# Performance work log

Measured on AMD Instinct MI355X. Metric: run time of the kernel, lower is better.

## Reference

```python
import jax, jax.numpy as jnp
import numpy as np
import math

D = 512          # model_dim
H = 8            # num_heads
HD = D // H      # head_dim
L = 6            # num_layers
FF = 2 * D       # dim_feedforward
IN_DIM = 24
MAX_LEN = 1024   # positional_embedding_dim (sinusoidal max_len)
NUM_CLASSES = 1
B, S = 8, 1024
EPS = 1e-5


def make_sinusoidal_pe(max_len, d_model):
    position = np.arange(max_len, dtype=np.float32)[:, None]
    div_term = np.exp(np.arange(0, d_model, 2, dtype=np.float32) * (-math.log(10000.0) / d_model))
    pe = np.zeros((max_len, d_model), dtype=np.float32)
    pe[:, 0::2] = np.sin(position * div_term)
    pe[:, 1::2] = np.cos(position * div_term)
    return jnp.asarray(pe)


def layer_norm(x, g, b):
    mu = jnp.mean(x, axis=-1, keepdims=True)
    var = jnp.mean(jnp.square(x - mu), axis=-1, keepdims=True)
    return (x - mu) * jax.lax.rsqrt(var + EPS) * g + b


def setup_inputs() -> dict:
    key = jax.random.key(0)
    ks = jax.random.split(key, 16)
    xavier = lambda k, shape: jax.random.uniform(
        k, shape, jnp.float32,
        -math.sqrt(6.0 / (shape[-2] + shape[-1])),
        math.sqrt(6.0 / (shape[-2] + shape[-1])))
    inp = {
        'x': jax.random.normal(ks[0], (B, S, IN_DIM), jnp.float32),
        'positions': jax.random.randint(ks[1], (B, S), 0, MAX_LEN),
        'pe': make_sinusoidal_pe(MAX_LEN, D),
        'input_W': xavier(ks[2], (IN_DIM, D)),
        'input_b': jnp.zeros((D,), jnp.float32),
        'qkv_W': xavier(ks[3], (L, D, 3 * D)),
        'qkv_b': jnp.zeros((L, 3 * D), jnp.float32),
        'o_W': xavier(ks[4], (L, D, D)),
        'o_b': jnp.zeros((L, D), jnp.float32),
        'ff1_W': xavier(ks[5], (L, D, FF)),
        'ff1_b': jnp.zeros((L, FF), jnp.float32),
        'ff2_W': xavier(ks[6], (L, FF, D)),
        'ff2_b': jnp.zeros((L, D), jnp.float32),
        'ln1_g': jnp.ones((L, D), jnp.float32),
        'ln1_b': jnp.zeros((L, D), jnp.float32),
        'ln2_g': jnp.ones((L, D), jnp.float32),
        'ln2_b': jnp.zeros((L, D), jnp.float32),
        'out1_W': xavier(ks[7], (D, D)),
        'out1_b': jnp.zeros((D,), jnp.float32),
        'outln_g': jnp.ones((D,), jnp.float32),
        'outln_b': jnp.zeros((D,), jnp.float32),
        'out2_W': xavier(ks[8], (D, NUM_CLASSES)),
        'out2_b': jnp.zeros((NUM_CLASSES,), jnp.float32),
    }
    return inp


def reference(x, positions, pe, input_W, input_b, qkv_W, qkv_b, o_W, o_b,
              ff1_W, ff1_b, ff2_W, ff2_b, ln1_g, ln1_b, ln2_g, ln2_b,
              out1_W, out1_b, outln_g, outln_b, out2_W, out2_b):
    b, s, _ = x.shape
    # input projection + sinusoidal positional encoding gathered at positions
    h = x @ input_W + input_b + pe[positions]            # [B,S,D]
    scale = 1.0 / math.sqrt(HD)
    for l in range(qkv_W.shape[0]):
        qkv = (h @ qkv_W[l] + qkv_b[l]).reshape(b, s, H, 3 * HD)
        q = jnp.transpose(qkv[..., :HD], (0, 2, 1, 3))           # [B,H,S,hd]
        k = jnp.transpose(qkv[..., HD:2 * HD], (0, 2, 1, 3))
        v = jnp.transpose(qkv[..., 2 * HD:], (0, 2, 1, 3))
        logits = jnp.einsum('bhqd,bhkd->bhqk', q, k) * scale     # [B,H,S,S]
        attn = jax.nn.softmax(logits, axis=-1)
        vals = jnp.einsum('bhqk,bhkd->bhqd', attn, v)
        vals = jnp.transpose(vals, (0, 2, 1, 3)).reshape(b, s, D)
        attn_out = vals @ o_W[l] + o_b[l]
        h = layer_norm(h + attn_out, ln1_g[l], ln1_b[l])
        ff = jax.nn.relu(h @ ff1_W[l] + ff1_b[l]) @ ff2_W[l] + ff2_b[l]
        h = layer_norm(h + ff, ln2_g[l], ln2_b[l])
    pooled = jnp.mean(h, axis=1)                                 # [B,D] mean pooling
    o = jax.nn.relu(layer_norm(pooled @ out1_W + out1_b, outln_g, outln_b))
    return o @ out2_W + out2_b                                   # [B,num_classes]
```

## Files before the change

### kernel.cpp

```cpp
#include <hip/hip_runtime.h>
#include <cstddef>

#define EPS 1e-5f

typedef short bf16x8 __attribute__((ext_vector_type(8)));
typedef float f32x4 __attribute__((ext_vector_type(4)));
typedef unsigned short u16x8 __attribute__((ext_vector_type(8)));
typedef unsigned short u16x4 __attribute__((ext_vector_type(4)));

__device__ __forceinline__ unsigned short f2bf(float x) {
  unsigned u = __float_as_uint(x);
  return (unsigned short)((u + 0x7FFFu + ((u >> 16) & 1u)) >> 16);
}

__device__ __forceinline__ void gl2lds16(const unsigned short* g, unsigned short* l) {
  __builtin_amdgcn_global_load_lds(
      (const __attribute__((address_space(1))) unsigned int*)g,
      (__attribute__((address_space(3))) unsigned int*)l, 16, 0, 0);
}

__global__ __launch_bounds__(512) void inproj_kernel(
    const float* __restrict__ x, const int* __restrict__ pos,
    const float* __restrict__ pe, const float* __restrict__ Wp,
    const float* __restrict__ bp, float* __restrict__ h,
    unsigned short* __restrict__ hb) {
  int t = blockIdx.x, d = threadIdx.x;
  __shared__ float xs[24];
  if (d < 24) xs[d] = x[(size_t)t * 24 + d];
  __syncthreads();
  float acc = bp[d] + pe[(size_t)pos[t] * 512 + d];
#pragma unroll
  for (int k = 0; k < 24; ++k) acc += xs[k] * Wp[k * 512 + d];
  h[(size_t)t * 512 + d] = acc;
  hb[(size_t)t * 512 + d] = f2bf(acc);
}

__global__ __launch_bounds__(256) void wcast_kernel(
    const float* __restrict__ qw, const float* __restrict__ ow,
    const float* __restrict__ f1w, const float* __restrict__ f2w,
    unsigned short* __restrict__ qd, unsigned short* __restrict__ od,
    unsigned short* __restrict__ f1d, unsigned short* __restrict__ f2d) {
  __shared__ float sm[64][65];
  int bid = blockIdx.x;
  const float* src; unsigned short* dst; int K, N, tile;
  if (bid < 192)      { src = qw;  dst = qd;  K = 512;  N = 1536; tile = bid; }
  else if (bid < 256) { src = ow;  dst = od;  K = 512;  N = 512;  tile = bid - 192; }
  else if (bid < 384) { src = f1w; dst = f1d; K = 512;  N = 1024; tile = bid - 256; }
  else                { src = f2w; dst = f2d; K = 1024; N = 512;  tile = bid - 384; }
  int nt = N >> 6;
  int tk = tile / nt, tn = tile % nt;
  int k0 = tk * 64, n0 = tn * 64;
  int tid = threadIdx.x;
#pragma unroll
  for (int it = 0; it < 16; ++it) {
    int idx = it * 256 + tid;
    int ki = idx >> 6, ni = idx & 63;
    sm[ki][ni] = src[(size_t)(k0 + ki) * N + n0 + ni];
  }
  __syncthreads();
#pragma unroll
  for (int it = 0; it < 16; ++it) {
    int idx = it * 256 + tid;
    int ni = idx >> 6, ki = idx & 63;
    dst[(size_t)(n0 + ni) * K + k0 + ki] = f2bf(sm[ki][ni]);
  }
}

template <int MODE>
__global__ __launch_bounds__(256) void gemm_bf16(
    const unsigned short* __restrict__ A, const unsigned short* __restrict__ Bw,
    const float* __restrict__ bias, float* __restrict__ Cf,
    unsigned short* __restrict__ Cb, unsigned short* __restrict__ q_out,
    unsigned short* __restrict__ k_out, unsigned short* __restrict__ v_out,
    int M, int N, int K) {
  __shared__ unsigned short As[128 * 64];
  __shared__ unsigned short Bs[128 * 64];
  int tid = threadIdx.x;
  int w = tid >> 6, l = tid & 63;
  int wm = w >> 1, wn = w & 1;
  int cl = l & 15, kg = l >> 4;
  int n0 = blockIdx.x * 128, m0 = blockIdx.y * 128;
  f32x4 acc[4][4];
#pragma unroll
  for (int i = 0; i < 4; ++i)
#pragma unroll
    for (int j = 0; j < 4; ++j) acc[i][j] = f32x4{0.f, 0.f, 0.f, 0.f};

  const unsigned short* Ap = A + (size_t)m0 * K;
  const unsigned short* Bp = Bw + (size_t)n0 * K;

  for (int k0 = 0; k0 < K; k0 += 64) {
    __syncthreads();
#pragma unroll
    for (int c = 0; c < 4; ++c) {
      int idx = c * 256 + tid;
      int r = idx >> 3;
      int kq = (idx & 7) ^ (r & 7);
      gl2lds16(Ap + (size_t)r * K + k0 + kq * 8, &As[(c * 256 + w * 64) * 8]);
    }
#pragma unroll
    for (int c = 0; c < 4; ++c) {
      int idx = c * 256 + tid;
      int r = idx >> 3;
      int kq = (idx & 7) ^ (r & 7);
      gl2lds16(Bp + (size_t)r * K + k0 + kq * 8, &Bs[(c * 256 + w * 64) * 8]);
    }
    __syncthreads();
    bf16x8 af[4][2], bfr[4][2];
    int key = (cl & 7) << 4;
#pragma unroll
    for (int i = 0; i < 4; ++i) {
      int rowa = wm * 64 + i * 16 + cl;
      int rowb = wn * 64 + i * 16 + cl;
#pragma unroll
      for (int s2 = 0; s2 < 2; ++s2) {
        af[i][s2]  = *(const bf16x8*)((char*)As + ((rowa * 128 + s2 * 64 + kg * 16) ^ key));
        bfr[i][s2] = *(const bf16x8*)((char*)Bs + ((rowb * 128 + s2 * 64 + kg * 16) ^ key));
      }
    }
#pragma unroll
    for (int i = 0; i < 4; ++i)
#pragma unroll
      for (int j = 0; j < 4; ++j) {
        acc[i][j] = __builtin_amdgcn_mfma_f32_16x16x32_bf16(af[i][0], bfr[j][0], acc[i][j], 0, 0, 0);
        acc[i][j] = __builtin_amdgcn_mfma_f32_16x16x32_bf16(af[i][1], bfr[j][1], acc[i][j], 0, 0, 0);
      }
  }

  int rl = kg * 4;
#pragma unroll
  for (int i = 0; i < 4; ++i) {
    int mbase = m0 + wm * 64 + i * 16 + rl;
#pragma unroll
    for (int j = 0; j < 4; ++j) {
      int col = n0 + wn * 64 + j * 16 + cl;
      float bv = bias[col];
      if (MODE == 0) {
#pragma unroll
        for (int r = 0; r < 4; ++r)
          Cf[(size_t)(mbase + r) * N + col] = acc[i][j][r] + bv;
      } else if (MODE == 1) {
#pragma unroll
        for (int r = 0; r < 4; ++r)
          Cb[(size_t)(mbase + r) * N + col] = f2bf(fmaxf(acc[i][j][r] + bv, 0.f));
      } else {
        int hh = col / 192;
        int rem = col - hh * 192;
        int which = rem >> 6, d = rem & 63;
        int b = mbase >> 10, s = mbase & 1023;
        if (which == 2) {
          u16x4 pk;
#pragma unroll
          for (int r = 0; r < 4; ++r) pk[r] = f2bf(acc[i][j][r] + bv);
          *(u16x4*)&v_out[((size_t)((b * 8 + hh) * 64 + d)) * 1024 + s] = pk;
        } else {
          unsigned short* dst = (which == 0) ? q_out : k_out;
#pragma unroll
          for (int r = 0; r < 4; ++r)
            dst[(((size_t)(b * 8 + hh)) * 1024 + s + r) * 64 + d] = f2bf(acc[i][j][r] + bv);
        }
      }
    }
  }
}

__global__ __launch_bounds__(512) void attn_mfma(
    const unsigned short* __restrict__ qT, const unsigned short* __restrict__ kT,
    const unsigned short* __restrict__ vT, unsigned short* __restrict__ valsb) {
  __shared__ unsigned short Ks[128 * 64];
  __shared__ unsigned short Vs[64 * 128];
  __shared__ unsigned short Ps[8][16 * 128];

  int bh = blockIdx.x >> 3;
  int qt = blockIdx.x & 7;
  int b = bh >> 3, h = bh & 7;
  int tid = threadIdx.x;
  int w = tid >> 6, l = tid & 63;
  int cl = l & 15, kg = l >> 4, rl = kg * 4;

  const unsigned short* kgb = kT + (size_t)bh * 65536;
  const unsigned short* vgb = vT + (size_t)bh * 65536;

  int q0 = qt * 128 + w * 16;
  const unsigned short* qbase = qT + ((size_t)bh * 1024 + q0) * 64;
  bf16x8 aq[2];
  aq[0] = *(const bf16x8*)(qbase + cl * 64 + kg * 8);
  aq[1] = *(const bf16x8*)(qbase + cl * 64 + 32 + kg * 8);

  int kk = tid >> 3, ka = tid & 7;
  int vd = tid >> 4, vs = tid & 15;
  int kb0 = (kk * 128 + ka * 16) ^ ((kk & 7) << 4);
  int kb1 = kb0 + 64 * 128;
  int vb0 = (vd * 256 + vs * 16) ^ ((vd & 7) << 4);
  int vb1 = vb0 + 32 * 256;

  const float C = 0.125f * 1.44269504f;
  float m2[4], lsum[4];
  f32x4 accO[4];
#pragma unroll
  for (int r = 0; r < 4; ++r) { m2[r] = -1e30f; lsum[r] = 0.f; }
#pragma unroll
  for (int df = 0; df < 4; ++df) accO[df] = f32x4{0.f, 0.f, 0.f, 0.f};

  char* Pw = (char*)&Ps[w][0];

  uint4 kr0 = *(const uint4*)(kgb + (size_t)kk * 64 + ka * 8);
  uint4 kr1 = *(const uint4*)(kgb + (size_t)(kk + 64) * 64 + ka * 8);
  uint4 vr0 = *(const uint4*)(vgb + (size_t)vd * 1024 + vs * 8);
  uint4 vr1 = *(const uint4*)(vgb + (size_t)(vd + 32) * 1024 + vs * 8);

  for (int c = 0; c < 8; ++c) {
    __syncthreads();
    *(uint4*)((char*)Ks + kb0) = kr0;
    *(uint4*)((char*)Ks + kb1) = kr1;
    *(uint4*)((char*)Vs + vb0) = vr0;
    *(uint4*)((char*)Vs + vb1) = vr1;
    if (c < 7) {
      kr0 = *(const uint4*)(kgb + (size_t)((c + 1) * 128 + kk) * 64 + ka * 8);
      kr1 = *(const uint4*)(kgb + (size_t)((c + 1) * 128 + kk + 64) * 64 + ka * 8);
      vr0 = *(const uint4*)(vgb + (size_t)vd * 1024 + (c + 1) * 128 + vs * 8);
      vr1 = *(const uint4*)(vgb + (size_t)(vd + 32) * 1024 + (c + 1) * 128 + vs * 8);
    }
    __syncthreads();

    f32x4 s[8];
    int keyq = (cl & 7) << 4;
#pragma unroll
    for (int kf = 0; kf < 8; ++kf) {
      s[kf] = f32x4{0.f, 0.f, 0.f, 0.f};
      int row = kf * 16 + cl;
#pragma unroll
      for (int ks = 0; ks < 2; ++ks) {
        int boff = (row * 128 + ks * 64 + kg * 16) ^ keyq;
        s[kf] = __builtin_amdgcn_mfma_f32_16x16x32_bf16(
            aq[ks], *(const bf16x8*)((char*)Ks + boff), s[kf], 0, 0, 0);
      }
    }

    float lmax[4];
#pragma unroll
    for (int r = 0; r < 4; ++r) {
      float a0 = fmaxf(fmaxf(s[0][r], s[1][r]), fmaxf(s[2][r], s[3][r]));
      float a1 = fmaxf(fmaxf(s[4][r], s[5][r]), fmaxf(s[6][r], s[7][r]));
      lmax[r] = fmaxf(a0, a1);
    }
    float need = fmaxf(fmaxf(lmax[0] * C - m2[0], lmax[1] * C - m2[1]),
                       fmaxf(lmax[2] * C - m2[2], lmax[3] * C - m2[3]));
    if (!__all(need <= 8.0f)) {
      float cm[4];
#pragma unroll
      for (int r = 0; r < 4; ++r) cm[r] = lmax[r];
#pragma unroll
      for (int off = 1; off < 16; off <<= 1)
#pragma unroll
        for (int r = 0; r < 4; ++r) cm[r] = fmaxf(cm[r], __shfl_xor(cm[r], off));
#pragma unroll
      for (int r = 0; r < 4; ++r) {
        float mn = fmaxf(m2[r], cm[r] * C);
        float alpha = exp2f(m2[r] - mn);
        m2[r] = mn;
        lsum[r] *= alpha;
        accO[0][r] *= alpha; accO[1][r] *= alpha;
        accO[2][r] *= alpha; accO[3][r] *= alpha;
      }
    }

#pragma unroll
    for (int kf = 0; kf < 8; ++kf) {
#pragma unroll
      for (int r = 0; r < 4; ++r) {
        float p = exp2f(s[kf][r] * C - m2[r]);
        lsum[r] += p;
        int row = rl + r;
        int boff = (row * 256 + (kf * 16 + cl) * 2) ^ ((row & 7) << 4);
        *(unsigned short*)(Pw + boff) =
            (unsigned short)((__float_as_uint(p) + 0x8000u) >> 16);
      }
    }

#pragma unroll
    for (int ks = 0; ks < 4; ++ks) {
      int pboff = (cl * 256 + ks * 64 + kg * 16) ^ ((cl & 7) << 4);
      bf16x8 ap = *(const bf16x8*)(Pw + pboff);
#pragma unroll
      for (int df = 0; df < 4; ++df) {
        int d = df * 16 + cl;
        int vboff = (d * 256 + ks * 64 + kg * 16) ^ ((d & 7) << 4);
        accO[df] = __builtin_amdgcn_mfma_f32_16x16x32_bf16(
            ap, *(const bf16x8*)((char*)Vs + vboff), accO[df], 0, 0, 0);
      }
    }
  }

#pragma unroll
  for (int off = 1; off < 16; off <<= 1)
#pragma unroll
    for (int r = 0; r < 4; ++r) lsum[r] += __shfl_xor(lsum[r], off);

  float inv[4];
#pragma unroll
  for (int r = 0; r < 4; ++r) inv[r] = 1.f / lsum[r];
#pragma unroll
  for (int df = 0; df < 4; ++df)
#pragma unroll
    for (int r = 0; r < 4; ++r) {
      int q = q0 + rl + r;
      int d = df * 16 + cl;
      valsb[(((size_t)b * 1024) + q) * 512 + h * 64 + d] = f2bf(accO[df][r] * inv[r]);
    }
}

__global__ __launch_bounds__(256) void ln_residual(
    float* __restrict__ h, const float* __restrict__ res,
    const float* __restrict__ g, const float* __restrict__ bb,
    unsigned short* __restrict__ hb) {
  int row = blockIdx.x * 4 + (threadIdx.x >> 6);
  int lane = threadIdx.x & 63;
  size_t base = (size_t)row * 512 + lane * 8;
  float4 v0 = *(const float4*)&h[base];
  float4 v1 = *(const float4*)&h[base + 4];
  float4 r0 = *(const float4*)&res[base];
  float4 r1 = *(const float4*)&res[base + 4];
  float xv[8];
  xv[0] = v0.x + r0.x; xv[1] = v0.y + r0.y; xv[2] = v0.z + r0.z; xv[3] = v0.w + r0.w;
  xv[4] = v1.x + r1.x; xv[5] = v1.y + r1.y; xv[6] = v1.z + r1.z; xv[7] = v1.w + r1.w;
  float s = 0.f, sq = 0.f;
#pragma unroll
  for (int i = 0; i < 8; ++i) { s += xv[i]; sq += xv[i] * xv[i]; }
#pragma unroll
  for (int off = 32; off; off >>= 1) { s += __shfl_xor(s, off); sq += __shfl_xor(sq, off); }
  float mu = s * (1.f / 512.f);
  float var = sq * (1.f / 512.f) - mu * mu;
  float rstd = rsqrtf(var + EPS);
  float4 g0 = *(const float4*)&g[lane * 8];
  float4 g1 = *(const float4*)&g[lane * 8 + 4];
  float4 b0 = *(const float4*)&bb[lane * 8];
  float4 b1 = *(const float4*)&bb[lane * 8 + 4];
  float o[8];
  o[0] = (xv[0] - mu) * rstd * g0.x + b0.x;
  o[1] = (xv[1] - mu) * rstd * g0.y + b0.y;
  o[2] = (xv[2] - mu) * rstd * g0.z + b0.z;
  o[3] = (xv[3] - mu) * rstd * g0.w + b0.w;
  o[4] = (xv[4] - mu) * rstd * g1.x + b1.x;
  o[5] = (xv[5] - mu) * rstd * g1.y + b1.y;
  o[6] = (xv[6] - mu) * rstd * g1.z + b1.z;
  o[7] = (xv[7] - mu) * rstd * g1.w + b1.w;
  *(float4*)&h[base] = make_float4(o[0], o[1], o[2], o[3]);
  *(float4*)&h[base + 4] = make_float4(o[4], o[5], o[6], o[7]);
  u16x8 hv;
#pragma unroll
  for (int i = 0; i < 8; ++i) hv[i] = f2bf(o[i]);
  *(u16x8*)&hb[base] = hv;
}

__global__ __launch_bounds__(512) void pool_kernel(
    const float* __restrict__ h, float* __restrict__ partial) {
  int b = blockIdx.x >> 3, c = blockIdx.x & 7, d = threadIdx.x;
  float s = 0.f;
  for (int t = 0; t < 128; ++t)
    s += h[((size_t)b * 1024 + c * 128 + t) * 512 + d];
  partial[(size_t)blockIdx.x * 512 + d] = s;
}

__global__ __launch_bounds__(512) void head_kernel(
    const float* __restrict__ partial, const float* __restrict__ W1,
    const float* __restrict__ b1, const float* __restrict__ g,
    const float* __restrict__ bb, const float* __restrict__ W2,
    const float* __restrict__ b2, float* __restrict__ out) {
  int b = blockIdx.x, tid = threadIdx.x;
  int wid = tid >> 6, lane = tid & 63;
  __shared__ float ps[512];
  __shared__ float red_s[8];
  __shared__ float red_q[8];
  float pv = 0.f;
#pragma unroll
  for (int c = 0; c < 8; ++c) pv += partial[((size_t)(b * 8 + c)) * 512 + tid];
  ps[tid] = pv * (1.f / 1024.f);
  __syncthreads();
  float acc = b1[tid];
  for (int k = 0; k < 512; ++k) acc += ps[k] * W1[(size_t)k * 512 + tid];
  float s = acc, sq = acc * acc;
#pragma unroll
  for (int off = 32; off; off >>= 1) { s += __shfl_xor(s, off); sq += __shfl_xor(sq, off); }
  if (lane == 0) { red_s[wid] = s; red_q[wid] = sq; }
  __syncthreads();
  float S = 0.f, Q = 0.f;
#pragma unroll
  for (int i = 0; i < 8; ++i) { S += red_s[i]; Q += red_q[i]; }
  float mu = S * (1.f / 512.f);
  float var = Q * (1.f / 512.f) - mu * mu;
  float rstd = rsqrtf(var + EPS);
  float z = (acc - mu) * rstd * g[tid] + bb[tid];
  float r = fmaxf(z, 0.f);
  float v = r * W2[tid];
#pragma unroll
  for (int off = 32; off; off >>= 1) v += __shfl_xor(v, off);
  __syncthreads();
  if (lane == 0) red_s[wid] = v;
  __syncthreads();
  if (tid == 0) {
    float t = 0.f;
#pragma unroll
    for (int i = 0; i < 8; ++i) t += red_s[i];
    out[b] = t + b2[0];
  }
}

extern "C" void kernel_launch(void* const* d_in, const int* in_sizes, int n_in,
                              void* d_out, int out_size, void* d_ws, size_t ws_size,
                              hipStream_t stream) {
  const float* x    = (const float*)d_in[0];
  const int*   pos  = (const int*)d_in[1];
  const float* pe   = (const float*)d_in[2];
  const float* inW  = (const float*)d_in[3];
  const float* inb  = (const float*)d_in[4];
  const float* qkvW = (const float*)d_in[5];
  const float* qkvb = (const float*)d_in[6];
  const float* oW   = (const float*)d_in[7];
  const float* ob   = (const float*)d_in[8];
  const float* f1W  = (const float*)d_in[9];
  const float* f1b  = (const float*)d_in[10];
  const float* f2W  = (const float*)d_in[11];
  const float* f2b  = (const float*)d_in[12];
  const float* l1g  = (const float*)d_in[13];
  const float* l1b  = (const float*)d_in[14];
  const float* l2g  = (const float*)d_in[15];
  const float* l2b  = (const float*)d_in[16];
  const float* o1W  = (const float*)d_in[17];
  const float* o1b  = (const float*)d_in[18];
  const float* og   = (const float*)d_in[19];
  const float* obb  = (const float*)d_in[20];
  const float* o2W  = (const float*)d_in[21];
  const float* o2b  = (const float*)d_in[22];
  float* out = (float*)d_out;

  char* W = (char*)d_ws;
  float*          h     = (float*)(W + 0);
  unsigned short* hb    = (unsigned short*)(W + 16777216);
  unsigned short* qTb   = (unsigned short*)(W + 25165824);
  unsigned short* kTb   = (unsigned short*)(W + 33554432);
  unsigned short* vTb   = (unsigned short*)(W + 41943040);
  unsigned short* valsb = (unsigned short*)(W + 50331648);
  float*          projf = (float*)(W + 25165824);
  unsigned short* ff1b  = (unsigned short*)(W + 41943040);
  unsigned short* wt    = (unsigned short*)(W + 58720256);
  float*          part  = (float*)(W + 62914560);

  unsigned short* wt_qkv = wt;
  unsigned short* wt_o   = wt + 786432;
  unsigned short* wt_f1  = wt + 1048576;
  unsigned short* wt_f2  = wt + 1572864;

  inproj_kernel<<<8192, 512, 0, stream>>>(x, pos, pe, inW, inb, h, hb);

  for (int l = 0; l < 6; ++l) {
    wcast_kernel<<<512, 256, 0, stream>>>(
        qkvW + (size_t)l * 512 * 1536, oW + (size_t)l * 512 * 512,
        f1W + (size_t)l * 512 * 1024, f2W + (size_t)l * 1024 * 512,
        wt_qkv, wt_o, wt_f1, wt_f2);

    gemm_bf16<2><<<dim3(12, 64), 256, 0, stream>>>(
        hb, wt_qkv, qkvb + l * 1536, nullptr, nullptr, qTb, kTb, vTb,
        8192, 1536, 512);

    attn_mfma<<<512, 512, 0, stream>>>(qTb, kTb, vTb, valsb);

    gemm_bf16<0><<<dim3(4, 64), 256, 0, stream>>>(
        valsb, wt_o, ob + l * 512, projf, nullptr, nullptr, nullptr, nullptr,
        8192, 512, 512);

    ln_residual<<<2048, 256, 0, stream>>>(h, projf, l1g + l * 512, l1b + l * 512, hb);

    gemm_bf16<1><<<dim3(8, 64), 256, 0, stream>>>(
        hb, wt_f1, f1b + l * 1024, nullptr, ff1b, nullptr, nullptr, nullptr,
        8192, 1024, 512);

    gemm_bf16<0><<<dim3(4, 64), 256, 0, stream>>>(
        ff1b, wt_f2, f2b + l * 512, projf, nullptr, nullptr, nullptr, nullptr,
        8192, 512, 1024);

    ln_residual<<<2048, 256, 0, stream>>>(h, projf, l2g + l * 512, l2b + l * 512, hb);
  }

  pool_kernel<<<64, 512, 0, stream>>>(h, part);
  head_kernel<<<8, 512, 0, stream>>>(part, o1W, o1b, og, obb, o2W, o2b, out);
}
```

Measured before the change: 1.156 ms.

## Double-buffer GEMM and attention LDS, shrink tiles, store projections as bf16

The GEMM and attention kernels now double-buffer their LDS tiles, so the next K/V or A/B tile streams in through global_load_lds while the current tile is multiplied, with one barrier per iteration instead of two. Attention moves to 256-thread blocks with 64-key chunks and a bh-major block order. The N=512 GEMMs use a 64-row M tile to launch more blocks. The output and FF2 projections are written as bf16 rather than fp32 to halve residual traffic into the layernorm, at a small cost in precision.

```diff
diff --git a/kernel.cpp b/kernel.cpp
--- a/kernel.cpp
+++ b/kernel.cpp
@@ -11,6 +11,9 @@
 __device__ __forceinline__ unsigned short f2bf(float x) {
   unsigned u = __float_as_uint(x);
   return (unsigned short)((u + 0x7FFFu + ((u >> 16) & 1u)) >> 16);
+}
+__device__ __forceinline__ float bf2f(unsigned short v) {
+  return __uint_as_float((unsigned)v << 16);
 }
 
 __device__ __forceinline__ void gl2lds16(const unsigned short* g, unsigned short* l) {
@@ -66,83 +69,95 @@
   }
 }
 
-template <int MODE>
+template <int MODE, int BM>
 __global__ __launch_bounds__(256) void gemm_bf16(
     const unsigned short* __restrict__ A, const unsigned short* __restrict__ Bw,
-    const float* __restrict__ bias, float* __restrict__ Cf,
+    const float* __restrict__ bias,
     unsigned short* __restrict__ Cb, unsigned short* __restrict__ q_out,
     unsigned short* __restrict__ k_out, unsigned short* __restrict__ v_out,
     int M, int N, int K) {
-  __shared__ unsigned short As[128 * 64];
-  __shared__ unsigned short Bs[128 * 64];
+  constexpr int MI = BM / 32;
+  __shared__ unsigned short As[2][BM * 64];
+  __shared__ unsigned short Bs[2][128 * 64];
   int tid = threadIdx.x;
   int w = tid >> 6, l = tid & 63;
   int wm = w >> 1, wn = w & 1;
   int cl = l & 15, kg = l >> 4;
-  int n0 = blockIdx.x * 128, m0 = blockIdx.y * 128;
-  f32x4 acc[4][4];
-#pragma unroll
-  for (int i = 0; i < 4; ++i)
+  int n0 = blockIdx.x * 128, m0 = blockIdx.y * BM;
+  f32x4 acc[MI][4];
+#pragma unroll
+  for (int i = 0; i < MI; ++i)
 #pragma unroll
     for (int j = 0; j < 4; ++j) acc[i][j] = f32x4{0.f, 0.f, 0.f, 0.f};
 
   const unsigned short* Ap = A + (size_t)m0 * K;
   const unsigned short* Bp = Bw + (size_t)n0 * K;
 
-  for (int k0 = 0; k0 < K; k0 += 64) {
-    __syncthreads();
-#pragma unroll
-    for (int c = 0; c < 4; ++c) {
-      int idx = c * 256 + tid;
+  auto stage = [&](int buf, int t) {
+#pragma unroll
+    for (int p = 0; p < BM / 32; ++p) {
+      int idx = p * 256 + tid;
       int r = idx >> 3;
       int kq = (idx & 7) ^ (r & 7);
-      gl2lds16(Ap + (size_t)r * K + k0 + kq * 8, &As[(c * 256 + w * 64) * 8]);
-    }
-#pragma unroll
-    for (int c = 0; c < 4; ++c) {
-      int idx = c * 256 + tid;
+      gl2lds16(Ap + (size_t)r * K + t * 64 + kq * 8, &As[buf][(p * 256 + w * 64) * 8]);
+    }
+#pragma unroll
+    for (int p = 0; p < 4; ++p) {
+      int idx = p * 256 + tid;
       int r = idx >> 3;
       int kq = (idx & 7) ^ (r & 7);
-      gl2lds16(Bp + (size_t)r * K + k0 + kq * 8, &Bs[(c * 256 + w * 64) * 8]);
-    }
-    __syncthreads();
-    bf16x8 af[4][2], bfr[4][2];
+      gl2lds16(Bp + (size_t)r * K + t * 64 + kq * 8, &Bs[buf][(p * 256 + w * 64) * 8]);
+    }
+  };
+
+  stage(0, 0);
+  __syncthreads();
+  int nk = K >> 6;
+  for (int t = 0; t < nk; ++t) {
+    int cur = t & 1;
+    if (t + 1 < nk) stage(cur ^ 1, t + 1);
+    bf16x8 af[MI][2], bfr[4][2];
     int key = (cl & 7) << 4;
 #pragma unroll
-    for (int i = 0; i < 4; ++i) {
-      int rowa = wm * 64 + i * 16 + cl;
-      int rowb = wn * 64 + i * 16 + cl;
-#pragma unroll
-      for (int s2 = 0; s2 < 2; ++s2) {
-        af[i][s2]  = *(const bf16x8*)((char*)As + ((rowa * 128 + s2 * 64 + kg * 16) ^ key));
-        bfr[i][s2] = *(const bf16x8*)((char*)Bs + ((rowb * 128 + s2 * 64 + kg * 16) ^ key));
-      }
-    }
-#pragma unroll
-    for (int i = 0; i < 4; ++i)
+    for (int i = 0; i < MI; ++i) {
+      int rowa = wm * (BM / 2) + i * 16 + cl;
+#pragma unroll
+      for (int s2 = 0; s2 < 2; ++s2)
+        af[i][s2] = *(const bf16x8*)((char*)As[cur] + ((rowa * 128 + s2 * 64 + kg * 16) ^ key));
+    }
+#pragma unroll
+    for (int j = 0; j < 4; ++j) {
+      int rowb = wn * 64 + j * 16 + cl;
+#pragma unroll
+      for (int s2 = 0; s2 < 2; ++s2)
+        bfr[j][s2] = *(const bf16x8*)((char*)Bs[cur] + ((rowb * 128 + s2 * 64 + kg * 16) ^ key));
+    }
+#pragma unroll
+    for (int i = 0; i < MI; ++i)
 #pragma unroll
       for (int j = 0; j < 4; ++j) {
         acc[i][j] = __builtin_amdgcn_mfma_f32_16x16x32_bf16(af[i][0], bfr[j][0], acc[i][j], 0, 0, 0);
         acc[i][j] = __builtin_amdgcn_mfma_f32_16x16x32_bf16(af[i][1], bfr[j][1], acc[i][j], 0, 0, 0);
       }
+    __syncthreads();
   }
 
   int rl = kg * 4;
 #pragma unroll
-  for (int i = 0; i < 4; ++i) {
-    int mbase = m0 + wm * 64 + i * 16 + rl;
+  for (int i = 0; i < MI; ++i) {
+    int mbase = m0 + wm * (BM / 2) + i * 16 + rl;
 #pragma unroll
     for (int j = 0; j < 4; ++j) {
       int col = n0 + wn * 64 + j * 16 + cl;
       float bv = bias[col];
-      if (MODE == 0) {
-#pragma unroll
-        for (int r = 0; r < 4; ++r)
-          Cf[(size_t)(mbase + r) * N + col] = acc[i][j][r] + bv;
-      } else if (MODE == 1) {
+      if (MODE == 1) {
 #pragma unroll
         for (int r = 0; r < 4; ++r)
           Cb[(size_t)(mbase + r) * N + col] = f2bf(fmaxf(acc[i][j][r] + bv, 0.f));
+      } else if (MODE == 3) {
+#pragma unroll
+        for (int r = 0; r < 4; ++r)
+          Cb[(size_t)(mbase + r) * N + col] = f2bf(acc[i][j][r] + bv);
       } else {
         int hh = col / 192;
         int rem = col - hh * 192;
@@ -164,15 +179,15 @@
   }
 }
 
-__global__ __launch_bounds__(512) void attn_mfma(
+__global__ __launch_bounds__(256) void attn_mfma(
     const unsigned short* __restrict__ qT, const unsigned short* __restrict__ kT,
     const unsigned short* __restrict__ vT, unsigned short* __restrict__ valsb) {
-  __shared__ unsigned short Ks[128 * 64];
-  __shared__ unsigned short Vs[64 * 128];
-  __shared__ unsigned short Ps[8][16 * 128];
-
-  int bh = blockIdx.x >> 3;
-  int qt = blockIdx.x & 7;
+  __shared__ unsigned short Ks[2][64 * 64];
+  __shared__ unsigned short Vs[2][64 * 64];
+  __shared__ unsigned short Ps[4][16 * 64];
+
+  int bh = blockIdx.x & 63;
+  int qt = blockIdx.x >> 6;
   int b = bh >> 3, h = bh & 7;
   int tid = threadIdx.x;
   int w = tid >> 6, l = tid & 63;
@@ -181,18 +196,28 @@
   const unsigned short* kgb = kT + (size_t)bh * 65536;
   const unsigned short* vgb = vT + (size_t)bh * 65536;
 
-  int q0 = qt * 128 + w * 16;
+  int q0 = qt * 64 + w * 16;
   const unsigned short* qbase = qT + ((size_t)bh * 1024 + q0) * 64;
   bf16x8 aq[2];
   aq[0] = *(const bf16x8*)(qbase + cl * 64 + kg * 8);
   aq[1] = *(const bf16x8*)(qbase + cl * 64 + 32 + kg * 8);
 
-  int kk = tid >> 3, ka = tid & 7;
-  int vd = tid >> 4, vs = tid & 15;
-  int kb0 = (kk * 128 + ka * 16) ^ ((kk & 7) << 4);
-  int kb1 = kb0 + 64 * 128;
-  int vb0 = (vd * 256 + vs * 16) ^ ((vd & 7) << 4);
-  int vb1 = vb0 + 32 * 256;
+  auto stage = [&](int buf, int c) {
+#pragma unroll
+    for (int p = 0; p < 2; ++p) {
+      int idx = p * 256 + tid;
+      int r = idx >> 3;
+      int kq = (idx & 7) ^ (r & 7);
+      gl2lds16(kgb + ((size_t)(c * 64 + r)) * 64 + kq * 8, &Ks[buf][(p * 256 + w * 64) * 8]);
+    }
+#pragma unroll
+    for (int p = 0; p < 2; ++p) {
+      int idx = p * 256 + tid;
+      int r = idx >> 3;
+      int kq = (idx & 7) ^ (r & 7);
+      gl2lds16(vgb + (size_t)r * 1024 + c * 64 + kq * 8, &Vs[buf][(p * 256 + w * 64) * 8]);
+    }
+  };
 
   const float C = 0.125f * 1.44269504f;
   float m2[4], lsum[4];
@@ -204,46 +229,30 @@
 
   char* Pw = (char*)&Ps[w][0];
 
-  uint4 kr0 = *(const uint4*)(kgb + (size_t)kk * 64 + ka * 8);
-  uint4 kr1 = *(const uint4*)(kgb + (size_t)(kk + 64) * 64 + ka * 8);
-  uint4 vr0 = *(const uint4*)(vgb + (size_t)vd * 1024 + vs * 8);
-  uint4 vr1 = *(const uint4*)(vgb + (size_t)(vd + 32) * 1024 + vs * 8);
-
-  for (int c = 0; c < 8; ++c) {
-    __syncthreads();
-    *(uint4*)((char*)Ks + kb0) = kr0;
-    *(uint4*)((char*)Ks + kb1) = kr1;
-    *(uint4*)((char*)Vs + vb0) = vr0;
-    *(uint4*)((char*)Vs + vb1) = vr1;
-    if (c < 7) {
-      kr0 = *(const uint4*)(kgb + (size_t)((c + 1) * 128 + kk) * 64 + ka * 8);
-      kr1 = *(const uint4*)(kgb + (size_t)((c + 1) * 128 + kk + 64) * 64 + ka * 8);
-      vr0 = *(const uint4*)(vgb + (size_t)vd * 1024 + (c + 1) * 128 + vs * 8);
-      vr1 = *(const uint4*)(vgb + (size_t)(vd + 32) * 1024 + (c + 1) * 128 + vs * 8);
-    }
-    __syncthreads();
-
-    f32x4 s[8];
-    int keyq = (cl & 7) << 4;
-#pragma unroll
-    for (int kf = 0; kf < 8; ++kf) {
+  stage(0, 0);
+  __syncthreads();
+
+  for (int c = 0; c < 16; ++c) {
+    int cur = c & 1;
+    if (c < 15) stage(cur ^ 1, c + 1);
+
+    f32x4 s[4];
+#pragma unroll
+    for (int kf = 0; kf < 4; ++kf) {
       s[kf] = f32x4{0.f, 0.f, 0.f, 0.f};
       int row = kf * 16 + cl;
 #pragma unroll
       for (int ks = 0; ks < 2; ++ks) {
-        int boff = (row * 128 + ks * 64 + kg * 16) ^ keyq;
+        int boff = (row * 128 + ks * 64 + kg * 16) ^ ((row & 7) << 4);
         s[kf] = __builtin_amdgcn_mfma_f32_16x16x32_bf16(
-            aq[ks], *(const bf16x8*)((char*)Ks + boff), s[kf], 0, 0, 0);
+            aq[ks], *(const bf16x8*)((char*)Ks[cur] + boff), s[kf], 0, 0, 0);
       }
     }
 
     float lmax[4];
 #pragma unroll
-    for (int r = 0; r < 4; ++r) {
-      float a0 = fmaxf(fmaxf(s[0][r], s[1][r]), fmaxf(s[2][r], s[3][r]));
-      float a1 = fmaxf(fmaxf(s[4][r], s[5][r]), fmaxf(s[6][r], s[7][r]));
-      lmax[r] = fmaxf(a0, a1);
-    }
+    for (int r = 0; r < 4; ++r)
+      lmax[r] = fmaxf(fmaxf(s[0][r], s[1][r]), fmaxf(s[2][r], s[3][r]));
     float need = fmaxf(fmaxf(lmax[0] * C - m2[0], lmax[1] * C - m2[1]),
                        fmaxf(lmax[2] * C - m2[2], lmax[3] * C - m2[3]));
     if (!__all(need <= 8.0f)) {
@@ -266,30 +275,32 @@
     }
 
 #pragma unroll
-    for (int kf = 0; kf < 8; ++kf) {
+    for (int kf = 0; kf < 4; ++kf) {
 #pragma unroll
       for (int r = 0; r < 4; ++r) {
         float p = exp2f(s[kf][r] * C - m2[r]);
         lsum[r] += p;
         int row = rl + r;
-        int boff = (row * 256 + (kf * 16 + cl) * 2) ^ ((row & 7) << 4);
+        int boff = (row * 128 + (kf * 16 + cl) * 2) ^ ((row & 7) << 4);
         *(unsigned short*)(Pw + boff) =
             (unsigned short)((__float_as_uint(p) + 0x8000u) >> 16);
       }
     }
 
 #pragma unroll
-    for (int ks = 0; ks < 4; ++ks) {
-      int pboff = (cl * 256 + ks * 64 + kg * 16) ^ ((cl & 7) << 4);
+    for (int ks = 0; ks < 2; ++ks) {
+      int pboff = (cl * 128 + ks * 64 + kg * 16) ^ ((cl & 7) << 4);
       bf16x8 ap = *(const bf16x8*)(Pw + pboff);
 #pragma unroll
       for (int df = 0; df < 4; ++df) {
         int d = df * 16 + cl;
-        int vboff = (d * 256 + ks * 64 + kg * 16) ^ ((d & 7) << 4);
+        int vboff = (d * 128 + ks * 64 + kg * 16) ^ ((d & 7) << 4);
         accO[df] = __builtin_amdgcn_mfma_f32_16x16x32_bf16(
-            ap, *(const bf16x8*)((char*)Vs + vboff), accO[df], 0, 0, 0);
-      }
-    }
+            ap, *(const bf16x8*)((char*)Vs[cur] + vboff), accO[df], 0, 0, 0);
+      }
+    }
+
+    __syncthreads();
   }
 
 #pragma unroll
@@ -311,7 +322,7 @@
 }
 
 __global__ __launch_bounds__(256) void ln_residual(
-    float* __restrict__ h, const float* __restrict__ res,
+    float* __restrict__ h, const unsigned short* __restrict__ res,
     const float* __restrict__ g, const float* __restrict__ bb,
     unsigned short* __restrict__ hb) {
   int row = blockIdx.x * 4 + (threadIdx.x >> 6);
@@ -319,11 +330,12 @@
   size_t base = (size_t)row * 512 + lane * 8;
   float4 v0 = *(const float4*)&h[base];
   float4 v1 = *(const float4*)&h[base + 4];
-  float4 r0 = *(const float4*)&res[base];
-  float4 r1 = *(const float4*)&res[base + 4];
+  u16x8 rv = *(const u16x8*)&res[base];
   float xv[8];
-  xv[0] = v0.x + r0.x; xv[1] = v0.y + r0.y; xv[2] = v0.z + r0.z; xv[3] = v0.w + r0.w;
-  xv[4] = v1.x + r1.x; xv[5] = v1.y + r1.y; xv[6] = v1.z + r1.z; xv[7] = v1.w + r1.w;
+  xv[0] = v0.x + bf2f(rv[0]); xv[1] = v0.y + bf2f(rv[1]);
+  xv[2] = v0.z + bf2f(rv[2]); xv[3] = v0.w + bf2f(rv[3]);
+  xv[4] = v1.x + bf2f(rv[4]); xv[5] = v1.y + bf2f(rv[5]);
+  xv[6] = v1.z + bf2f(rv[6]); xv[7] = v1.w + bf2f(rv[7]);
   float s = 0.f, sq = 0.f;
 #pragma unroll
   for (int i = 0; i < 8; ++i) { s += xv[i]; sq += xv[i] * xv[i]; }
@@ -441,7 +453,7 @@
   unsigned short* kTb   = (unsigned short*)(W + 33554432);
   unsigned short* vTb   = (unsigned short*)(W + 41943040);
   unsigned short* valsb = (unsigned short*)(W + 50331648);
-  float*          projf = (float*)(W + 25165824);
+  unsigned short* projb = (unsigned short*)(W + 25165824);
   unsigned short* ff1b  = (unsigned short*)(W + 41943040);
   unsigned short* wt    = (unsigned short*)(W + 58720256);
   float*          part  = (float*)(W + 62914560);
@@ -459,27 +471,23 @@
         f1W + (size_t)l * 512 * 1024, f2W + (size_t)l * 1024 * 512,
         wt_qkv, wt_o, wt_f1, wt_f2);
 
-    gemm_bf16<2><<<dim3(12, 64), 256, 0, stream>>>(
-        hb, wt_qkv, qkvb + l * 1536, nullptr, nullptr, qTb, kTb, vTb,
-        8192, 1536, 512);
-
-    attn_mfma<<<512, 512, 0, stream>>>(qTb, kTb, vTb, valsb);
-
-    gemm_bf16<0><<<dim3(4, 64), 256, 0, stream>>>(
-        valsb, wt_o, ob + l * 512, projf, nullptr, nullptr, nullptr, nullptr,
-        8192, 512, 512);
-
-    ln_residual<<<2048, 256, 0, stream>>>(h, projf, l1g + l * 512, l1b + l * 512, hb);
-
-    gemm_bf16<1><<<dim3(8, 64), 256, 0, stream>>>(
-        hb, wt_f1, f1b + l * 1024, nullptr, ff1b, nullptr, nullptr, nullptr,
-        8192, 1024, 512);
-
-    gemm_bf16<0><<<dim3(4, 64), 256, 0, stream>>>(
-        ff1b, wt_f2, f2b + l * 512, projf, nullptr, nullptr, nullptr, nullptr,
-        8192, 512, 1024);
-
-    ln_residual<<<2048, 256, 0, stream>>>(h, projf, l2g + l * 512, l2b + l * 512, hb);
+    gemm_bf16<2, 128><<<dim3(12, 64), 256, 0, stream>>>(
+        hb, wt_qkv, qkvb + l * 1536, nullptr, qTb, kTb, vTb, 8192, 1536, 512);
+
+    attn_mfma<<<1024, 256, 0, stream>>>(qTb, kTb, vTb, valsb);
+
+    gemm_bf16<3, 64><<<dim3(4, 128), 256, 0, stream>>>(
+        valsb, wt_o, ob + l * 512, projb, nullptr, nullptr, nullptr, 8192, 512, 512);
+
+    ln_residual<<<2048, 256, 0, stream>>>(h, projb, l1g + l * 512, l1b + l * 512, hb);
+
+    gemm_bf16<1, 128><<<dim3(8, 64), 256, 0, stream>>>(
+        hb, wt_f1, f1b + l * 1024, ff1b, nullptr, nullptr, nullptr, 8192, 1024, 512);
+
+    gemm_bf16<3, 64><<<dim3(4, 128), 256, 0, stream>>>(
+        ff1b, wt_f2, f2b + l * 512, projb, nullptr, nullptr, nullptr, 8192, 512, 1024);
+
+    ln_residual<<<2048, 256, 0, stream>>>(h, projb, l2g + l * 512, l2b + l * 512, hb);
   }
 
   pool_kernel<<<64, 512, 0, stream>>>(h, part);
```

Result: faster. 1.023 ms (-11.5%).
